# Kernel tuning notes

Measured on AMD Instinct MI355X. Metric: run time of the kernel, lower is better.

## Reference

```python
import jax, jax.numpy as jnp
import numpy as np
import math

H, D, DEG = 8, 64, 2
GATE_BIAS = 6.906768

def _rope(x, sin, cos):
    # GPT-J style interleaved rotary: even lanes = x1*cos - x2*sin, odd = x2*cos + x1*sin
    x1, x2 = x[..., ::2], x[..., 1::2]
    s = sin[None, :, None, :]
    c = cos[None, :, None, :]
    even = x1 * c - x2 * s
    odd = x2 * c + x1 * s
    return jnp.stack([even, odd], axis=-1).reshape(x.shape)

def _forward(x, w_attn, w_proj):
    B, T, C = x.shape
    h, d, deg = H, D, DEG
    hd = h * d
    scale = 1.0 / math.sqrt(d)
    qkvg = x @ w_attn                                   # (B,T,3hd+h)
    q = qkvg[..., :hd].reshape(B, T, h, d)
    k = qkvg[..., hd:2 * hd].reshape(B, T, h, d)
    v = qkvg[..., 2 * hd:3 * hd].reshape(B, T, h, d)
    log_g = jax.nn.log_sigmoid(GATE_BIAS + qkvg[..., 3 * hd:].astype(jnp.float32))  # (B,T,h)
    # sinusoidal RoPE with frequency 2*pi / T**(2i/d), as in get_sinusoidal_embeddings
    pos = jnp.arange(T, dtype=jnp.float32)
    div = 2.0 * math.pi / (float(T) ** (jnp.arange(0, d, 2, dtype=jnp.float32) / d))
    ang = pos[:, None] * div[None, :]                   # (T, d//2)
    sin, cos = jnp.sin(ang), jnp.cos(ang)
    q = _rope(q, sin, cos)
    k = _rope(k, sin, cos)
    # gated symmetric-power attention: quadratic reference of chunked power_full
    # score_ts = (scale * q_t . k_s)^deg * exp(L_t - L_s), causal, row-normalized
    L = jnp.cumsum(log_g, axis=1).transpose(0, 2, 1)    # (B,h,T) cumulative log-gates
    qk = jnp.einsum('bthd,bshd->bhts', q, k) * scale    # (B,h,T,T)
    log_gate = L[:, :, :, None] - L[:, :, None, :]      # L_t - L_s
    causal = jnp.tril(jnp.ones((T, T), dtype=bool))
    scores = jnp.where(causal, (qk ** deg) * jnp.exp(log_gate), 0.0)
    denom = jnp.maximum(scores.sum(-1, keepdims=True), 1e-6)
    y = jnp.einsum('bhts,bshd->bthd', scores / denom, v)  # (B,T,h,d)
    return y.reshape(B, T, hd) @ w_proj

def setup_inputs() -> dict:
    key = jax.random.key(0)
    k1, k2, k3 = jax.random.split(key, 3)
    B, T, C = 2, 2048, 512
    x = jax.random.normal(k1, (B, T, C), dtype=jnp.float32)
    w_attn = jax.random.normal(k2, (C, 3 * H * D + H), dtype=jnp.float32) * 0.02
    w_proj = jax.random.normal(k3, (H * D, C), dtype=jnp.float32) * 0.02
    return {"x": x, "w_attn": w_attn, "w_proj": w_proj}

def reference(x, w_attn, w_proj):
    return _forward(x, w_attn, w_proj)
```

## Files before the change

kernel.cpp:

```cpp
#include <hip/hip_runtime.h>
#include <math.h>

constexpr int B_ = 2, T_ = 2048, C_ = 512, H_ = 8, D_ = 64;
constexpr int QKVG_ = 3 * H_ * D_ + H_;
constexpr float GATE_BIAS_ = 6.906768f;
constexpr int NPAD1_ = 1664;
constexpr int SC_ = 8;
constexpr int NBLK_ = 1280;
constexpr int MC_ = 4096 * 512;
constexpr int BHT_ = B_ * H_ * T_;

typedef __attribute__((ext_vector_type(8))) short short8;
typedef __attribute__((ext_vector_type(4))) float f32x4;

__device__ __forceinline__ unsigned short f2b(float f) {
    unsigned int u = __float_as_uint(f);
    unsigned int r = (u + 0x7fffu + ((u >> 16) & 1u)) >> 16;
    return (unsigned short)r;
}
__device__ __forceinline__ short8 pack8(float4 a, float4 b) {
    short8 r;
    r[0] = (short)f2b(a.x); r[1] = (short)f2b(a.y);
    r[2] = (short)f2b(a.z); r[3] = (short)f2b(a.w);
    r[4] = (short)f2b(b.x); r[5] = (short)f2b(b.y);
    r[6] = (short)f2b(b.z); r[7] = (short)f2b(b.w);
    return r;
}

__device__ __forceinline__ void packT_body(
    const float* __restrict__ W, unsigned short* __restrict__ Bt,
    int K, int N, int nt, int kt, int tid, float (*Ws)[65])
{
    {
        const int r = tid >> 2;
        const int c0 = (tid & 3) * 16;
#pragma unroll
        for (int j = 0; j < 16; ++j) {
            const int n = nt + c0 + j;
            Ws[r][c0 + j] = (n < N) ? W[(size_t)(kt + r) * N + n] : 0.f;
        }
    }
    __syncthreads();
    {
        const int d = tid >> 2;
        const int kc = (tid & 3) * 16;
        short8 o0, o1;
#pragma unroll
        for (int j = 0; j < 8; ++j) o0[j] = (short)f2b(Ws[kc + j][d]);
#pragma unroll
        for (int j = 0; j < 8; ++j) o1[j] = (short)f2b(Ws[kc + 8 + j][d]);
        unsigned short* op = Bt + (size_t)(nt + d) * K + kt + kc;
        *(short8*)(op + 0) = o0;
        *(short8*)(op + 8) = o1;
    }
}

__global__ __launch_bounds__(256) void pack_inputs(
    const float* __restrict__ x, const float* __restrict__ w_attn,
    const float* __restrict__ w_proj, unsigned short* __restrict__ xb,
    unsigned short* __restrict__ Bt1, unsigned short* __restrict__ Bt2)
{
    __shared__ float Ws[64][65];
    const int bid = blockIdx.x;
    const int tid = threadIdx.x;
    if (bid < 1024) {
        const int i = bid * 256 + tid;
        float4 f0 = *(const float4*)(x + (size_t)i * 8);
        float4 f1 = *(const float4*)(x + (size_t)i * 8 + 4);
        *(short8*)(xb + (size_t)i * 8) = pack8(f0, f1);
    } else if (bid < 1232) {
        const int q = bid - 1024;
        packT_body(w_attn, Bt1, C_, QKVG_, (q % 26) * 64, (q / 26) * 64, tid, Ws);
    } else {
        const int q = bid - 1232;
        packT_body(w_proj, Bt2, H_ * D_, C_, (q & 7) * 64, (q >> 3) * 64, tid, Ws);
    }
}

__global__ __launch_bounds__(256) void gemm_bf16(
    const unsigned short* __restrict__ A, const unsigned short* __restrict__ Bt,
    float* __restrict__ C, int M, int N, int K)
{
    __shared__ __align__(16) char AsB[128 * 128];
    __shared__ __align__(16) char BsB[128 * 128];

    const int tid = threadIdx.x;
    const int wave = tid >> 6, lane = tid & 63;
    const int l15 = lane & 15, lhi = lane >> 4;
    const int wr = wave >> 1, wc = wave & 1;
    const int bm = blockIdx.y * 128, bn = blockIdx.x * 128;

    f32x4 acc[4][4];
#pragma unroll
    for (int i = 0; i < 4; ++i)
#pragma unroll
        for (int j = 0; j < 4; ++j) acc[i][j] = (f32x4){0.f, 0.f, 0.f, 0.f};

    const unsigned short* Arow = A + (size_t)bm * K;
    const unsigned short* Brow = Bt + (size_t)bn * K;
    const int sw = (l15 & 7) << 4;

    for (int k0 = 0; k0 < K; k0 += 64) {
        __syncthreads();
#pragma unroll
        for (int p = 0; p < 4; ++p) {
            const int idx = p * 256 + tid;
            const int row = idx >> 3;
            const int kc = (idx & 7) * 8;
            const int ldso = row * 128 + ((kc * 2) ^ ((row & 7) << 4));
            *(short8*)(AsB + ldso) = *(const short8*)(Arow + (size_t)row * K + k0 + kc);
            *(short8*)(BsB + ldso) = *(const short8*)(Brow + (size_t)row * K + k0 + kc);
        }
        __syncthreads();

        short8 af[4][2];
#pragma unroll
        for (int mi = 0; mi < 4; ++mi) {
            const int row = wr * 64 + mi * 16 + l15;
#pragma unroll
            for (int kk = 0; kk < 2; ++kk)
                af[mi][kk] = *(const short8*)(AsB + row * 128 + ((kk * 64 + lhi * 16) ^ sw));
        }
#pragma unroll
        for (int ni = 0; ni < 4; ++ni) {
            const int row = wc * 64 + ni * 16 + l15;
            short8 bf0 = *(const short8*)(BsB + row * 128 + ((lhi * 16) ^ sw));
            short8 bf1 = *(const short8*)(BsB + row * 128 + ((64 + lhi * 16) ^ sw));
#pragma unroll
            for (int mi = 0; mi < 4; ++mi) {
                acc[mi][ni] = __builtin_amdgcn_mfma_f32_16x16x32_bf16(af[mi][0], bf0, acc[mi][ni], 0, 0, 0);
                acc[mi][ni] = __builtin_amdgcn_mfma_f32_16x16x32_bf16(af[mi][1], bf1, acc[mi][ni], 0, 0, 0);
            }
        }
    }

#pragma unroll
    for (int mi = 0; mi < 4; ++mi) {
        const int gm = bm + wr * 64 + mi * 16 + lhi * 4;
#pragma unroll
        for (int r = 0; r < 4; ++r) {
            float* crow = C + (size_t)(gm + r) * N;
#pragma unroll
            for (int ni = 0; ni < 4; ++ni) {
                const int gn = bn + wc * 64 + ni * 16 + l15;
                if (gn < N) crow[gn] = acc[mi][ni][r];
            }
        }
    }
}

__global__ __launch_bounds__(256) void gate_cumsum(
    const float* __restrict__ qkvg, float* __restrict__ Lg)
{
    __shared__ float wsum[4];
    const int bh = blockIdx.x;
    const int b = bh >> 3, h = bh & 7;
    const int tid = threadIdx.x;
    const int lane = tid & 63, wv = tid >> 6;

    const float* gp = qkvg + (size_t)(b * T_ + tid * 8) * QKVG_ + 1536 + h;
    float v[8];
    float s = 0.f;
#pragma unroll
    for (int j = 0; j < 8; ++j) {
        const float z = gp[(size_t)j * QKVG_] + GATE_BIAS_;
        const float lg = (z > 0.f) ? -log1pf(expf(-z)) : (z - log1pf(expf(z)));
        s += lg;
        v[j] = s;
    }
    float ssum = s;
#pragma unroll
    for (int off = 1; off < 64; off <<= 1) {
        float n = __shfl_up(ssum, off, 64);
        if (lane >= off) ssum += n;
    }
    if (lane == 63) wsum[wv] = ssum;
    __syncthreads();
    float base = ssum - s;
#pragma unroll
    for (int w = 0; w < 3; ++w)
        base += (w < wv) ? wsum[w] : 0.f;

    float* op = Lg + (size_t)bh * T_ + tid * 8;
#pragma unroll
    for (int j = 0; j < 8; ++j) op[j] = v[j] + base;
}

__global__ __launch_bounds__(256) void qkv_pack(
    const float* __restrict__ qkvg, const float* __restrict__ Lg,
    unsigned short* __restrict__ Qsb, unsigned short* __restrict__ Ksb,
    unsigned short* __restrict__ Vtb)
{
    __shared__ float Vs[64][68];
    const int tid = threadIdx.x;
    const int stile = blockIdx.x;
    const int bh = blockIdx.y;
    const int b = bh >> 3, h = bh & 7;
    const int r = tid >> 2, c = tid & 3;
    const int t = stile * 64 + r;

    float sn[8], cs[8];
#pragma unroll
    for (int j = 0; j < 8; ++j) {
        const int i = c * 8 + j;
        const float div = 6.2831853071795864f * exp2f((float)i * (-11.0f / 32.0f));
        const float ang = (float)t * div;
        sn[j] = sinf(ang);
        cs[j] = cosf(ang);
    }

    const float Lt = Lg[(size_t)bh * T_ + t];
    const float eQ = __expf(0.5f * Lt) * 0.125f;
    const float eK = __expf(-0.5f * Lt);
    const float* basep = qkvg + (size_t)(b * T_ + t) * QKVG_ + h * 64 + c * 16;

    {
        float q[16];
        *(float4*)&q[0]  = *(const float4*)(basep + 0);
        *(float4*)&q[4]  = *(const float4*)(basep + 4);
        *(float4*)&q[8]  = *(const float4*)(basep + 8);
        *(float4*)&q[12] = *(const float4*)(basep + 12);
#pragma unroll
        for (int j = 0; j < 8; ++j) {
            const float x1 = q[2 * j], x2 = q[2 * j + 1];
            q[2 * j]     = (x1 * cs[j] - x2 * sn[j]) * eQ;
            q[2 * j + 1] = (x2 * cs[j] + x1 * sn[j]) * eQ;
        }
        unsigned short* op = Qsb + ((size_t)bh * T_ + t) * 64 + c * 16;
        *(short8*)(op + 0) = pack8(*(float4*)&q[0], *(float4*)&q[4]);
        *(short8*)(op + 8) = pack8(*(float4*)&q[8], *(float4*)&q[12]);
    }
    {
        float k[16];
        *(float4*)&k[0]  = *(const float4*)(basep + 512);
        *(float4*)&k[4]  = *(const float4*)(basep + 516);
        *(float4*)&k[8]  = *(const float4*)(basep + 520);
        *(float4*)&k[12] = *(const float4*)(basep + 524);
#pragma unroll
        for (int j = 0; j < 8; ++j) {
            const float x1 = k[2 * j], x2 = k[2 * j + 1];
            k[2 * j]     = (x1 * cs[j] - x2 * sn[j]) * eK;
            k[2 * j + 1] = (x2 * cs[j] + x1 * sn[j]) * eK;
        }
        unsigned short* op = Ksb + ((size_t)bh * T_ + t) * 64 + c * 16;
        *(short8*)(op + 0) = pack8(*(float4*)&k[0], *(float4*)&k[4]);
        *(short8*)(op + 8) = pack8(*(float4*)&k[8], *(float4*)&k[12]);
    }
    {
        *(float4*)&Vs[r][c * 16 + 0]  = *(const float4*)(basep + 1024);
        *(float4*)&Vs[r][c * 16 + 4]  = *(const float4*)(basep + 1028);
        *(float4*)&Vs[r][c * 16 + 8]  = *(const float4*)(basep + 1032);
        *(float4*)&Vs[r][c * 16 + 12] = *(const float4*)(basep + 1036);
    }
    __syncthreads();
    {
        const int d = tid >> 2, cc = tid & 3;
        short8 o0, o1;
#pragma unroll
        for (int j = 0; j < 8; ++j) o0[j] = (short)f2b(Vs[cc * 16 + j][d]);
#pragma unroll
        for (int j = 0; j < 8; ++j) o1[j] = (short)f2b(Vs[cc * 16 + 8 + j][d]);
        unsigned short* op = Vtb + ((size_t)bh * 64 + d) * T_ + stile * 64 + cc * 16;
        *(short8*)(op + 0) = o0;
        *(short8*)(op + 8) = o1;
    }
}

__global__ __launch_bounds__(256) void attn_mfma(
    const unsigned short* __restrict__ Qsb, const unsigned short* __restrict__ Ksb,
    const unsigned short* __restrict__ Vtb,
    float* __restrict__ Y0, float* __restrict__ Yp, float* __restrict__ Dpart)
{
    __shared__ __align__(16) char smem[24576];
    char* KsB = smem;
    char* VtB = smem + 8192;
    char* PsB = smem + 16384;

    const int wg = blockIdx.x;
    const int xcd = wg & 7;
    const int slot = wg >> 3;
    const int bh = (slot < 80) ? xcd : 8 + xcd;
    const int rem = (slot < 80) ? slot : slot - 80;
    const int rr = 79 - rem;
    int bt, sc;
    if (rr < 8)       { bt = rr; sc = 0; }
    else if (rr < 24) { const int q = rr - 8;  bt = 8 + (q >> 1);  sc = q & 1; }
    else if (rr < 48) { const int q = rr - 24; bt = 16 + q / 3;    sc = q % 3; }
    else              { const int q = rr - 48; bt = 24 + (q >> 2); sc = q & 3; }
    const int st0 = sc * SC_;
    const int st1 = min(st0 + SC_ - 1, bt);

    const int tid = threadIdx.x;
    const int wave = tid >> 6;
    const int lane = tid & 63;
    const int l15 = lane & 15;
    const int lhi = lane >> 4;
    const int b = bh >> 3, h = bh & 7;
    const int t0 = bt * 64;

    const int qrow = t0 + wave * 16 + l15;
    const unsigned short* qpp = Qsb + ((size_t)bh * T_ + qrow) * 64 + lhi * 8;
    short8 qf[2];
    qf[0] = *(const short8*)(qpp);
    qf[1] = *(const short8*)(qpp + 32);

    f32x4 accY[4];
#pragma unroll
    for (int n = 0; n < 4; ++n) accY[n] = (f32x4){0.f, 0.f, 0.f, 0.f};
    float den[4] = {0.f, 0.f, 0.f, 0.f};

    const int kchunk = lhi * 16;
    const int rsw = (l15 & 7) << 4;
    const int srow = tid >> 2;
    const int c2 = (tid & 3) * 2;
    const int swr = (srow & 7) << 4;

    for (int st = st0; st <= st1; ++st) {
        __syncthreads();
        {
            const unsigned short* kp = Ksb + ((size_t)bh * T_ + st * 64 + srow) * 64 + c2 * 8;
            short8 k0 = *(const short8*)kp;
            short8 k1 = *(const short8*)(kp + 8);
            *(short8*)(KsB + srow * 128 + ((c2 * 16) ^ swr))      = k0;
            *(short8*)(KsB + srow * 128 + ((c2 * 16 + 16) ^ swr)) = k1;
            const unsigned short* vp = Vtb + ((size_t)bh * 64 + srow) * T_ + st * 64 + c2 * 8;
            short8 v0 = *(const short8*)vp;
            short8 v1 = *(const short8*)(vp + 8);
            *(short8*)(VtB + srow * 128 + ((c2 * 16) ^ swr))      = v0;
            *(short8*)(VtB + srow * 128 + ((c2 * 16 + 16) ^ swr)) = v1;
        }
        __syncthreads();

        f32x4 accS[4];
#pragma unroll
        for (int n = 0; n < 4; ++n) accS[n] = (f32x4){0.f, 0.f, 0.f, 0.f};
#pragma unroll
        for (int n = 0; n < 4; ++n) {
#pragma unroll
            for (int kk = 0; kk < 2; ++kk) {
                short8 bf = *(const short8*)(KsB + (n * 16 + l15) * 128 + ((kk * 64 + kchunk) ^ rsw));
                accS[n] = __builtin_amdgcn_mfma_f32_16x16x32_bf16(qf[kk], bf, accS[n], 0, 0, 0);
            }
        }

        const bool last = (st == bt);
        char* PsW = PsB + wave * 2048;
#pragma unroll
        for (int n = 0; n < 4; ++n) {
#pragma unroll
            for (int r = 0; r < 4; ++r) {
                const float a = accS[n][r];
                float p = a * a;
                if (last)
                    p = ((n * 16 + l15) <= wave * 16 + lhi * 4 + r) ? p : 0.f;
                den[r] += p;
                const int prow = lhi * 4 + r;
                *(unsigned short*)(PsW + prow * 128 + ((2 * (n * 16 + l15)) ^ ((prow & 7) << 4))) = f2b(p);
            }
        }

        short8 pa[2];
#pragma unroll
        for (int kk = 0; kk < 2; ++kk)
            pa[kk] = *(const short8*)(PsW + l15 * 128 + ((kk * 64 + kchunk) ^ rsw));
#pragma unroll
        for (int n = 0; n < 4; ++n) {
#pragma unroll
            for (int kk = 0; kk < 2; ++kk) {
                short8 vb = *(const short8*)(VtB + (n * 16 + l15) * 128 + ((kk * 64 + kchunk) ^ rsw));
                accY[n] = __builtin_amdgcn_mfma_f32_16x16x32_bf16(pa[kk], vb, accY[n], 0, 0, 0);
            }
        }
    }

#pragma unroll
    for (int r = 0; r < 4; ++r) {
        den[r] += __shfl_xor(den[r], 1, 64);
        den[r] += __shfl_xor(den[r], 2, 64);
        den[r] += __shfl_xor(den[r], 4, 64);
        den[r] += __shfl_xor(den[r], 8, 64);
    }

    float* Ybase = (sc == 0) ? Y0 : (Yp + (size_t)(sc - 1) * MC_);
    float* Dbase = Dpart + (size_t)sc * BHT_;
#pragma unroll
    for (int r = 0; r < 4; ++r) {
        const int t = t0 + wave * 16 + lhi * 4 + r;
        if (l15 == 0)
            Dbase[(size_t)bh * T_ + t] = den[r];
        float* yo = Ybase + (size_t)(b * T_ + t) * (H_ * D_) + h * 64 + l15;
#pragma unroll
        for (int n = 0; n < 4; ++n)
            yo[n * 16] = accY[n][r];
    }
}

__global__ __launch_bounds__(256) void normalize_kernel(
    const float* __restrict__ Y0, const float* __restrict__ Yp,
    const float* __restrict__ Dpart, unsigned short* __restrict__ ybb)
{
    const int gid = blockIdx.x * 256 + threadIdx.x;
    const size_t base = (size_t)gid * 8;
    const int row = (int)(base >> 9);
    const int col = (int)(base & 511);
    const int b = row >> 11, t = row & 2047, h = col >> 6;
    const int bh = b * H_ + h;
    const int nsc = ((t >> 6) >> 3) + 1;

    float d = Dpart[(size_t)bh * T_ + t];
    float4 f0 = *(const float4*)(Y0 + base);
    float4 f1 = *(const float4*)(Y0 + base + 4);
    for (int s = 1; s < nsc; ++s) {
        d += Dpart[(size_t)s * BHT_ + (size_t)bh * T_ + t];
        const float* yp = Yp + (size_t)(s - 1) * MC_ + base;
        float4 g0 = *(const float4*)(yp);
        float4 g1 = *(const float4*)(yp + 4);
        f0.x += g0.x; f0.y += g0.y; f0.z += g0.z; f0.w += g0.w;
        f1.x += g1.x; f1.y += g1.y; f1.z += g1.z; f1.w += g1.w;
    }
    const float inv = 1.0f / fmaxf(d, 1e-6f);
    f0.x *= inv; f0.y *= inv; f0.z *= inv; f0.w *= inv;
    f1.x *= inv; f1.y *= inv; f1.z *= inv; f1.w *= inv;
    *(short8*)(ybb + base) = pack8(f0, f1);
}

extern "C" void kernel_launch(void* const* d_in, const int* in_sizes, int n_in,
                              void* d_out, int out_size, void* d_ws, size_t ws_size,
                              hipStream_t stream)
{
    const float* x      = (const float*)d_in[0];
    const float* w_attn = (const float*)d_in[1];
    const float* w_proj = (const float*)d_in[2];
    float* out = (float*)d_out;

    float* qkvg = (float*)d_ws;
    float* Lg    = qkvg + (size_t)B_ * T_ * QKVG_;
    float* Dpart = Lg + BHT_;
    unsigned short* Vtb = (unsigned short*)(Dpart + 4 * BHT_);
    unsigned short* Bt1 = Vtb + (size_t)B_ * H_ * D_ * T_;
    unsigned short* Bt2 = Bt1 + (size_t)NPAD1_ * C_;
    unsigned short* xb  = Bt2 + (size_t)C_ * C_;
    unsigned short* Ksb = xb;
    unsigned short* ybb = xb;
    float* Yp = (float*)(xb + (size_t)MC_);
    unsigned short* Qsb = (unsigned short*)(Yp + 3 * (size_t)MC_);

    const int M = B_ * T_;

    pack_inputs<<<1296, 256, 0, stream>>>(x, w_attn, w_proj, xb, Bt1, Bt2);

    gemm_bf16<<<dim3(NPAD1_ / 128, M / 128), 256, 0, stream>>>(
        xb, Bt1, qkvg, M, QKVG_, C_);

    gate_cumsum<<<B_ * H_, 256, 0, stream>>>(qkvg, Lg);

    qkv_pack<<<dim3(T_ / 64, B_ * H_), 256, 0, stream>>>(qkvg, Lg, Qsb, Ksb, Vtb);

    attn_mfma<<<NBLK_, 256, 0, stream>>>(Qsb, Ksb, Vtb, out, Yp, Dpart);

    normalize_kernel<<<(MC_ / 8) / 256, 256, 0, stream>>>(out, Yp, Dpart, ybb);

    gemm_bf16<<<dim3(C_ / 128, M / 128), 256, 0, stream>>>(
        ybb, Bt2, out, M, C_, H_ * D_);
}
```

Before: 90.05 us.

## Use direct global-to-LDS loads with pre-swizzled producer layouts

Replaces the register-staged global→LDS copies in the GEMM and attention kernels with global_load_lds 16-byte direct loads. Because these loads write LDS linearly, the XOR swizzle is moved into the producers (xb, Bt packing, K, V transpose, ybb), which now write 16-byte chunks in pre-swizzled order in global memory. This is meant to cut VGPR traffic and instruction count for tile staging. The cost is coupling every producer's layout to the consumer's swizzle, and any mismatch would silently corrupt results.

```diff
diff --git a/kernel.cpp b/kernel.cpp
--- a/kernel.cpp
+++ b/kernel.cpp
@@ -27,6 +27,12 @@
     return r;
 }
 
+__device__ __forceinline__ void gl2lds16(const unsigned short* g, void* lds_base) {
+    __builtin_amdgcn_global_load_lds(
+        (const __attribute__((address_space(1))) unsigned int*)g,
+        (__attribute__((address_space(3))) unsigned int*)lds_base, 16, 0, 0);
+}
+
 __device__ __forceinline__ void packT_body(
     const float* __restrict__ W, unsigned short* __restrict__ Bt,
     int K, int N, int nt, int kt, int tid, float (*Ws)[65])
@@ -43,15 +49,17 @@
     __syncthreads();
     {
         const int d = tid >> 2;
-        const int kc = (tid & 3) * 16;
+        const int cc = tid & 3;
+        const int kc = cc * 16;
         short8 o0, o1;
 #pragma unroll
         for (int j = 0; j < 8; ++j) o0[j] = (short)f2b(Ws[kc + j][d]);
 #pragma unroll
         for (int j = 0; j < 8; ++j) o1[j] = (short)f2b(Ws[kc + 8 + j][d]);
-        unsigned short* op = Bt + (size_t)(nt + d) * K + kt + kc;
-        *(short8*)(op + 0) = o0;
-        *(short8*)(op + 8) = o1;
+        const int row = nt + d;
+        unsigned short* op = Bt + (size_t)row * K + kt;
+        *(short8*)(op + ((2 * cc) ^ (row & 7)) * 8)     = o0;
+        *(short8*)(op + ((2 * cc + 1) ^ (row & 7)) * 8) = o1;
     }
 }
 
@@ -67,7 +75,10 @@
         const int i = bid * 256 + tid;
         float4 f0 = *(const float4*)(x + (size_t)i * 8);
         float4 f1 = *(const float4*)(x + (size_t)i * 8 + 4);
-        *(short8*)(xb + (size_t)i * 8) = pack8(f0, f1);
+        const int row = i >> 6;
+        const int ic = i & 63;
+        const int swc = (ic & ~7) | ((ic & 7) ^ (row & 7));
+        *(short8*)(xb + (size_t)row * 512 + swc * 8) = pack8(f0, f1);
     } else if (bid < 1232) {
         const int q = bid - 1024;
         packT_body(w_attn, Bt1, C_, QKVG_, (q % 26) * 64, (q / 26) * 64, tid, Ws);
@@ -100,16 +111,17 @@
     const unsigned short* Brow = Bt + (size_t)bn * K;
     const int sw = (l15 & 7) << 4;
 
+    const int srow = tid >> 3;
+    const int schunk = tid & 7;
+
     for (int k0 = 0; k0 < K; k0 += 64) {
         __syncthreads();
 #pragma unroll
         for (int p = 0; p < 4; ++p) {
-            const int idx = p * 256 + tid;
-            const int row = idx >> 3;
-            const int kc = (idx & 7) * 8;
-            const int ldso = row * 128 + ((kc * 2) ^ ((row & 7) << 4));
-            *(short8*)(AsB + ldso) = *(const short8*)(Arow + (size_t)row * K + k0 + kc);
-            *(short8*)(BsB + ldso) = *(const short8*)(Brow + (size_t)row * K + k0 + kc);
+            const int row = p * 32 + srow;
+            const size_t goff = (size_t)row * K + k0 + schunk * 8;
+            gl2lds16(Arow + goff, AsB + p * 4096 + wave * 1024);
+            gl2lds16(Brow + goff, BsB + p * 4096 + wave * 1024);
         }
         __syncthreads();
 
@@ -242,9 +254,9 @@
             k[2 * j]     = (x1 * cs[j] - x2 * sn[j]) * eK;
             k[2 * j + 1] = (x2 * cs[j] + x1 * sn[j]) * eK;
         }
-        unsigned short* op = Ksb + ((size_t)bh * T_ + t) * 64 + c * 16;
-        *(short8*)(op + 0) = pack8(*(float4*)&k[0], *(float4*)&k[4]);
-        *(short8*)(op + 8) = pack8(*(float4*)&k[8], *(float4*)&k[12]);
+        unsigned short* op = Ksb + ((size_t)bh * T_ + t) * 64;
+        *(short8*)(op + ((2 * c) ^ (t & 7)) * 8)     = pack8(*(float4*)&k[0], *(float4*)&k[4]);
+        *(short8*)(op + ((2 * c + 1) ^ (t & 7)) * 8) = pack8(*(float4*)&k[8], *(float4*)&k[12]);
     }
     {
         *(float4*)&Vs[r][c * 16 + 0]  = *(const float4*)(basep + 1024);
@@ -260,9 +272,9 @@
         for (int j = 0; j < 8; ++j) o0[j] = (short)f2b(Vs[cc * 16 + j][d]);
 #pragma unroll
         for (int j = 0; j < 8; ++j) o1[j] = (short)f2b(Vs[cc * 16 + 8 + j][d]);
-        unsigned short* op = Vtb + ((size_t)bh * 64 + d) * T_ + stile * 64 + cc * 16;
-        *(short8*)(op + 0) = o0;
-        *(short8*)(op + 8) = o1;
+        unsigned short* op = Vtb + ((size_t)bh * 64 + d) * T_ + stile * 64;
+        *(short8*)(op + ((2 * cc) ^ (d & 7)) * 8)     = o0;
+        *(short8*)(op + ((2 * cc + 1) ^ (d & 7)) * 8) = o1;
     }
 }
 
@@ -311,23 +323,18 @@
 
     const int kchunk = lhi * 16;
     const int rsw = (l15 & 7) << 4;
-    const int srow = tid >> 2;
-    const int c2 = (tid & 3) * 2;
-    const int swr = (srow & 7) << 4;
+    const int srow = tid >> 3;
+    const int schunk = tid & 7;
 
     for (int st = st0; st <= st1; ++st) {
         __syncthreads();
-        {
-            const unsigned short* kp = Ksb + ((size_t)bh * T_ + st * 64 + srow) * 64 + c2 * 8;
-            short8 k0 = *(const short8*)kp;
-            short8 k1 = *(const short8*)(kp + 8);
-            *(short8*)(KsB + srow * 128 + ((c2 * 16) ^ swr))      = k0;
-            *(short8*)(KsB + srow * 128 + ((c2 * 16 + 16) ^ swr)) = k1;
-            const unsigned short* vp = Vtb + ((size_t)bh * 64 + srow) * T_ + st * 64 + c2 * 8;
-            short8 v0 = *(const short8*)vp;
-            short8 v1 = *(const short8*)(vp + 8);
-            *(short8*)(VtB + srow * 128 + ((c2 * 16) ^ swr))      = v0;
-            *(short8*)(VtB + srow * 128 + ((c2 * 16 + 16) ^ swr)) = v1;
+#pragma unroll
+        for (int p = 0; p < 2; ++p) {
+            const int row = p * 32 + srow;
+            gl2lds16(Ksb + ((size_t)bh * T_ + st * 64 + row) * 64 + schunk * 8,
+                     KsB + p * 4096 + wave * 1024);
+            gl2lds16(Vtb + ((size_t)bh * 64 + row) * T_ + st * 64 + schunk * 8,
+                     VtB + p * 4096 + wave * 1024);
         }
         __syncthreads();
 
@@ -421,7 +428,10 @@
     const float inv = 1.0f / fmaxf(d, 1e-6f);
     f0.x *= inv; f0.y *= inv; f0.z *= inv; f0.w *= inv;
     f1.x *= inv; f1.y *= inv; f1.z *= inv; f1.w *= inv;
-    *(short8*)(ybb + base) = pack8(f0, f1);
+
+    const int ic = col >> 3;
+    const int swc = (ic & ~7) | ((ic & 7) ^ (row & 7));
+    *(short8*)(ybb + (size_t)row * 512 + swc * 8) = pack8(f0, f1);
 }
 
 extern "C" void kernel_launch(void* const* d_in, const int* in_sizes, int n_in,
```

Result: no change. 89.60 us (-0.5%).
